# Kernel tuning notes

Hardware: AMD Instinct MI355X
Metric: run time of the kernel (lower is better)

## Reference

```python
import jax, jax.numpy as jnp
import numpy as np

N_PTS = 16384
DIM = 3

def setup_inputs() -> dict:
    key = jax.random.key(0)
    k1, k2 = jax.random.split(key)
    source_cloud = jax.random.normal(k1, (1, N_PTS, DIM), dtype=jnp.float32)
    target_cloud = jax.random.normal(k2, (1, N_PTS, DIM), dtype=jnp.float32)
    return {"source_cloud": source_cloud, "target_cloud": target_cloud}


def _min_sq_dists(x, y):
    # x: [B, N, D], y: [B, M, D] -> [B, N] squared distance to nearest neighbor in y
    x2 = jnp.sum(x * x, axis=-1)              # [B, N]
    y2 = jnp.sum(y * y, axis=-1)              # [B, M]
    xy = jnp.einsum('bnd,bmd->bnm', x, y)     # [B, N, M]
    d = x2[:, :, None] + y2[:, None, :] - 2.0 * xy  # squared dists, as pytorch3d knn_points
    return jnp.min(d, axis=-1)                # K=1 nearest neighbor


def reference(source_cloud, target_cloud):
    chamfer_forward = _min_sq_dists(source_cloud, target_cloud)[0]   # [N]
    chamfer_backward = _min_sq_dists(target_cloud, source_cloud)[0]  # [M]
    return (chamfer_forward, chamfer_backward)
```

## Files before the change

### kernel.cpp

```cpp
#include <hip/hip_runtime.h>

#define NPTS 16384
#define KS   16
#define BT   256
#define BROWS 128
#define TSPLIT 8
#define SWEEP (NPTS / TSPLIT)
#define NTILE (SWEEP / 32)

typedef __attribute__((ext_vector_type(8)))  short bf16x8;
typedef __attribute__((ext_vector_type(16))) float f32x16;
typedef __attribute__((ext_vector_type(8)))  unsigned short ushort8;

__device__ __forceinline__ unsigned short btrunc(float f) {
    return (unsigned short)(__float_as_uint(f) >> 16);
}
__device__ __forceinline__ float btruncf(float f) {
    return __uint_as_float(__float_as_uint(f) & 0xFFFF0000u);
}

__global__ void chamfer_pack(const float* __restrict__ s,
                             const float* __restrict__ t,
                             unsigned short* __restrict__ Apack,
                             unsigned short* __restrict__ Bpack,
                             float* __restrict__ sq,
                             unsigned* __restrict__ outinit)
{
    int i = blockIdx.x * blockDim.x + threadIdx.x;
    if (i >= 2 * NPTS) return;
    outinit[i] = 0x7F7F7F7Fu;
    int cloud = i >> 14;
    int p = i & (NPTS - 1);
    const float* base = cloud ? t : s;
    float x = base[3 * p], y = base[3 * p + 1], z = base[3 * p + 2];

    float xh = btruncf(x), yh = btruncf(y), zh = btruncf(z);
    float xl = x - xh, yl = y - yh, zl = z - zh;
    float q = x * x + y * y + z * z;
    float qh = btruncf(q), ql = q - qh;

    const unsigned short one = btrunc(1.0f);
    ushort8 A0 = { btrunc(-2.f * xh), btrunc(-2.f * xl), btrunc(-2.f * xh),
                   btrunc(-2.f * yh), btrunc(-2.f * yl), btrunc(-2.f * yh),
                   btrunc(-2.f * zh), btrunc(-2.f * zl) };
    ushort8 A1 = { btrunc(-2.f * zh), one, one, 0, 0, 0, 0, 0 };
    ushort8 B0 = { btrunc(xh), btrunc(xh), btrunc(xl),
                   btrunc(yh), btrunc(yh), btrunc(yl),
                   btrunc(zh), btrunc(zh) };
    ushort8 B1 = { btrunc(zl), btrunc(qh), btrunc(ql), 0, 0, 0, 0, 0 };

    *(ushort8*)(Apack + (size_t)i * KS)     = A0;
    *(ushort8*)(Apack + (size_t)i * KS + 8) = A1;
    *(ushort8*)(Bpack + (size_t)i * KS)     = B0;
    *(ushort8*)(Bpack + (size_t)i * KS + 8) = B1;
    sq[i] = q;
}

__global__ __launch_bounds__(BT, 8)
void chamfer_mfma(const unsigned short* __restrict__ Apack,
                  const unsigned short* __restrict__ Bpack,
                  const float* __restrict__ sq,
                  unsigned* __restrict__ out)
{
    const int dir = blockIdx.z;
    const unsigned short* A = Apack + (size_t)(dir ? NPTS : 0) * KS;
    const unsigned short* B = Bpack + (size_t)(dir ? 0 : NPTS) * KS;
    const float* s2 = sq + (dir ? NPTS : 0);
    unsigned* o = out + dir * NPTS;

    const int lane = threadIdx.x & 63;
    const int wv   = threadIdx.x >> 6;
    const int n32  = lane & 31;
    const int kh   = lane >> 5;

    const int rbase = blockIdx.x * BROWS + wv * 32;
    const bf16x8 a0 = *(const bf16x8*)(A + (size_t)(rbase + n32) * KS + kh * 8);

    f32x16 mn, zc;
#pragma unroll
    for (int r = 0; r < 16; ++r) { mn[r] = 1e30f; zc[r] = 0.0f; }

    const unsigned short* Bl = B + (size_t)(blockIdx.y * SWEEP + n32) * KS + kh * 8;

    for (int t = 0; t < NTILE; ++t) {
        bf16x8 b = *(const bf16x8*)(Bl + (size_t)t * 32 * KS);
        f32x16 c = __builtin_amdgcn_mfma_f32_32x32x16_bf16(a0, b, zc, 0, 0, 0);
#pragma unroll
        for (int k = 0; k < 16; ++k) mn[k] = fminf(mn[k], c[k]);
    }

#pragma unroll
    for (int r = 0; r < 16; ++r) {
        float v0 = mn[r];
        v0 = fminf(v0, __shfl_xor(v0, 1, 32));
        v0 = fminf(v0, __shfl_xor(v0, 2, 32));
        v0 = fminf(v0, __shfl_xor(v0, 4, 32));
        v0 = fminf(v0, __shfl_xor(v0, 8, 32));
        v0 = fminf(v0, __shfl_xor(v0, 16, 32));
        mn[r] = v0;
    }

    if (n32 == 0) {
#pragma unroll
        for (int r = 0; r < 16; ++r) {
            int row = rbase + (r & 3) + 8 * (r >> 2) + 4 * kh;
            float d = fmaxf(mn[r] + s2[row], 0.0f);
            atomicMin(&o[row], __float_as_uint(d));
        }
    }
}

extern "C" void kernel_launch(void* const* d_in, const int* in_sizes, int n_in,
                              void* d_out, int out_size, void* d_ws, size_t ws_size,
                              hipStream_t stream) {
    const float* s = (const float*)d_in[0];
    const float* t = (const float*)d_in[1];

    unsigned short* Apack = (unsigned short*)d_ws;
    unsigned short* Bpack = Apack + (size_t)2 * NPTS * KS;
    float* sq = (float*)(Bpack + (size_t)2 * NPTS * KS);

    chamfer_pack<<<(2 * NPTS + BT - 1) / BT, BT, 0, stream>>>(
        s, t, Apack, Bpack, sq, (unsigned*)d_out);

    dim3 grid(NPTS / BROWS, TSPLIT, 2);
    chamfer_mfma<<<grid, BT, 0, stream>>>(Apack, Bpack, sq, (unsigned*)d_out);
}
```

Baseline: 38.40 us.

## Software-pipeline B tile loads and issue paired MFMAs via inline asm

Halves the target split so each block sweeps twice as many tiles, and restructures the inner loop into phases of two back-to-back MFMAs issued with inline asm. The min-reduction is folded across both results, while the next tiles' B fragments are prefetched into registers two phases ahead. The aim is to hide global load latency and cut per-tile loop overhead. In exchange it uses fixed s_nop padding, sched barriers and higher register pressure (launch bounds lowered to 4 waves per EU), and produces fewer blocks and fewer atomics.

```diff
diff --git a/kernel.cpp b/kernel.cpp
--- a/kernel.cpp
+++ b/kernel.cpp
@@ -4,9 +4,10 @@
 #define KS   16
 #define BT   256
 #define BROWS 128
-#define TSPLIT 8
+#define TSPLIT 4
 #define SWEEP (NPTS / TSPLIT)
 #define NTILE (SWEEP / 32)
+#define NP (NTILE / 2)
 
 typedef __attribute__((ext_vector_type(8)))  short bf16x8;
 typedef __attribute__((ext_vector_type(16))) float f32x16;
@@ -56,7 +57,7 @@
     sq[i] = q;
 }
 
-__global__ __launch_bounds__(BT, 8)
+__global__ __launch_bounds__(BT, 4)
 void chamfer_mfma(const unsigned short* __restrict__ Apack,
                   const unsigned short* __restrict__ Bpack,
                   const float* __restrict__ sq,
@@ -76,18 +77,45 @@
     const int rbase = blockIdx.x * BROWS + wv * 32;
     const bf16x8 a0 = *(const bf16x8*)(A + (size_t)(rbase + n32) * KS + kh * 8);
 
-    f32x16 mn, zc;
+    f32x16 mn;
 #pragma unroll
-    for (int r = 0; r < 16; ++r) { mn[r] = 1e30f; zc[r] = 0.0f; }
+    for (int r = 0; r < 16; ++r) mn[r] = 1e30f;
 
     const unsigned short* Bl = B + (size_t)(blockIdx.y * SWEEP + n32) * KS + kh * 8;
+#define BTILE(t) (*(const bf16x8*)(Bl + (size_t)(t) * 32 * KS))
 
-    for (int t = 0; t < NTILE; ++t) {
-        bf16x8 b = *(const bf16x8*)(Bl + (size_t)t * 32 * KS);
-        f32x16 c = __builtin_amdgcn_mfma_f32_32x32x16_bf16(a0, b, zc, 0, 0, 0);
-#pragma unroll
-        for (int k = 0; k < 16; ++k) mn[k] = fminf(mn[k], c[k]);
+#define PHASE(bb0, bb1)                                                          \
+    {                                                                            \
+        f32x16 c0, c1;                                                           \
+        asm volatile("v_mfma_f32_32x32x16_bf16 %0, %2, %3, 0\n\t"                \
+                     "v_mfma_f32_32x32x16_bf16 %1, %2, %4, 0\n\t"                \
+                     "s_nop 7\n\ts_nop 7\n\ts_nop 7"                             \
+                     : "=&v"(c0), "=&v"(c1)                                      \
+                     : "v"(a0), "v"(bb0), "v"(bb1));                             \
+        __builtin_amdgcn_sched_barrier(0);                                       \
+        _Pragma("unroll")                                                        \
+        for (int k = 0; k < 16; ++k)                                             \
+            mn[k] = fminf(fminf(mn[k], c0[k]), c1[k]);        \
+        __builtin_amdgcn_sched_barrier(0);                                       \
+        asm volatile("" : "+v"(mn));   \
     }
+
+    bf16x8 x0 = BTILE(0), x1 = BTILE(1);
+    bf16x8 y0 = BTILE(2), y1 = BTILE(3);
+
+#pragma unroll 1
+    for (int p = 0; p < NP; p += 2) {
+        int ta = (2 * p + 4 < NTILE) ? 2 * p + 4 : NTILE - 2;
+        int tb = (2 * p + 6 < NTILE) ? 2 * p + 6 : NTILE - 2;
+        bf16x8 nx0 = BTILE(ta), nx1 = BTILE(ta + 1);
+        PHASE(x0, x1);
+        x0 = nx0; x1 = nx1;
+        bf16x8 ny0 = BTILE(tb), ny1 = BTILE(tb + 1);
+        PHASE(y0, y1);
+        y0 = ny0; y1 = ny1;
+    }
+#undef PHASE
+#undef BTILE
 
 #pragma unroll
     for (int r = 0; r < 16; ++r) {
```

After: 35.07 us. 8.7% less time.
